# Kernel tuning notes

Measured on AMD Instinct MI355X. Metric: run time of the kernel, lower is better.

The kernel has to match this reference:

```python
import jax, jax.numpy as jnp
import numpy as np

P = 7      # local_patch_size
H = 6      # heads
DH = 30    # dim_head


def setup_inputs() -> dict:
    key = jax.random.key(0)
    ks = jax.random.split(key, 5)
    b, dim, L = 16, 180, 14336
    inner = H * DH  # 180
    fmap = jax.random.normal(ks[0], (b, dim, L), dtype=jnp.float32)
    Wq = jax.random.normal(ks[1], (inner, dim), dtype=jnp.float32) * 0.05
    Wkv = jax.random.normal(ks[2], (2 * inner, dim), dtype=jnp.float32) * 0.05
    Wo = jax.random.normal(ks[3], (dim, inner), dtype=jnp.float32) * 0.05
    bo = jax.random.normal(ks[4], (dim,), dtype=jnp.float32) * 0.05
    return {"fmap": fmap, "Wq": Wq, "Wkv": Wkv, "Wo": Wo, "bo": bo}


def reference(fmap, Wq, Wkv, Wo, bo):
    b, c, L = fmap.shape
    l = L // P
    scale = DH ** -0.5
    # 'b c (l p) -> b c l p' windows
    x = fmap.reshape(b, c, l, P)
    # pointwise (kernel-1) conv projections
    q = jnp.einsum('ec,bclp->belp', Wq, x)
    kv = jnp.einsum('ec,bclp->belp', Wkv, x)
    k, v = jnp.split(kv, 2, axis=1)

    def split_heads(t):
        # (b, h*d, l, p) -> (b, l, h, p, d)
        return t.reshape(b, H, DH, l, P).transpose(0, 3, 1, 4, 2)

    q, k, v = map(split_heads, (q, k, v))
    dots = jnp.einsum('blhid,blhjd->blhij', q, k) * scale  # per-window 7x7 scores
    attn = jax.nn.softmax(dots, axis=-1)
    out = jnp.einsum('blhij,blhjd->blhid', attn, v)  # (b, l, h, p, d)
    # '(b l h) p d -> b (h d) (l p)'
    out = out.transpose(0, 2, 4, 1, 3).reshape(b, H * DH, l * P)
    return jnp.einsum('oe,bel->bol', Wo, out) + bo[None, :, None]
```

## Files before the change

### kernel.cpp

```cpp
#include <hip/hip_runtime.h>
#include <stdint.h>

namespace {

constexpr int DIM  = 180;
constexpr int LL   = 14336;
constexpr int B    = 16;
constexpr int T    = 56;
constexpr int NCH  = 256;
constexpr int EQKV = 540;

constexpr int QTS  = 392;
constexpr int KOFF = 192;
constexpr int QT_U16  = T * QTS;
constexpr int VT_U16  = 24 * 512;
constexpr int XSS     = 200;
constexpr int XS_U16  = 32 * XSS;
constexpr int LDS_U16 = QT_U16 + VT_U16 + XS_U16;

typedef __attribute__((ext_vector_type(8))) short bf16x8;
typedef __attribute__((ext_vector_type(4))) float f32x4;

union Frag { bf16x8 v; uint32_t u[4]; unsigned short s[8]; };

__device__ __forceinline__ unsigned short f2b(float f) {
  uint32_t u = __builtin_bit_cast(uint32_t, f);
  u = (u + 0x7fffu + ((u >> 16) & 1u)) >> 16;
  return (unsigned short)u;
}
__device__ __forceinline__ uint32_t pack2(float lo, float hi) {
  return (uint32_t)f2b(lo) | ((uint32_t)f2b(hi) << 16);
}
__device__ __forceinline__ f32x4 zero4() { f32x4 z = {0.f,0.f,0.f,0.f}; return z; }

}

__global__ __launch_bounds__(1024) void la_prep(
    const float* __restrict__ Wq, const float* __restrict__ Wkv,
    const float* __restrict__ Wo, unsigned short* __restrict__ wqkv_b,
    unsigned short* __restrict__ wo_h) {
  const int idx = (int)(blockIdx.x * 1024 + threadIdx.x);
  if (idx < 576 * 192) {
    const int e = idx / 192, c = idx - e * 192;
    float v = 0.f;
    if (e < EQKV && c < DIM)
      v = (e < DIM) ? Wq[e * DIM + c] : Wkv[(size_t)(e - DIM) * DIM + c];
    wqkv_b[idx] = f2b(v);
  } else {
    const int k = idx - 576 * 192;
    if (k < 192 * 192) {
      const int o = k / 192, cc = k - o * 192;
      const int h = cc >> 5, d = cc & 31;
      float v = 0.f;
      if (o < DIM && d < 30) v = Wo[o * DIM + h * 30 + d];
      wo_h[k] = f2b(v);
    }
  }
}

__global__ __launch_bounds__(512, 4) void la_main(
    const float* __restrict__ fmap, const unsigned short* __restrict__ wqkv,
    const unsigned short* __restrict__ wo_h, const float* __restrict__ bo,
    float* __restrict__ out) {
  __shared__ __align__(16) unsigned short lds[LDS_U16];
  unsigned short* qt = lds;
  unsigned short* vt = lds + QT_U16;
  unsigned short* xs = lds + QT_U16 + VT_U16;

  const int tid  = (int)threadIdx.x;
  const int wave = tid >> 6;
  const int lane = tid & 63;
  const int l15  = lane & 15;
  const int g    = lane >> 4;

  const int bi    = (int)blockIdx.x;
  const int b     = bi >> 8;
  const int chunk = bi & 255;
  const int t0    = chunk * T;

  const unsigned short* wA = wqkv + (size_t)l15 * 192 + g * 8;

#pragma unroll
  for (int it = 0; it < 3; ++it)
    ((uint4*)vt)[tid + it * 512] = make_uint4(0u, 0u, 0u, 0u);

#pragma unroll
  for (int ph = 0; ph < 2; ++ph) {
    const int tb = ph * 32;
#pragma unroll
    for (int it = 0; it < 3; ++it) {
      const int idx = tid + it * 512;
      const int c  = idx >> 3;
      const int tq = (idx & 7) * 4;
      float4 v = {0.f, 0.f, 0.f, 0.f};
      if (c < DIM && (tb + tq) < T)
        v = *(const float4*)(fmap + (size_t)(b * DIM + c) * LL + t0 + tb + tq);
      unsigned short* xr = xs + tq * XSS + c;
      xr[0 * XSS] = f2b(v.x);
      xr[1 * XSS] = f2b(v.y);
      xr[2 * XSS] = f2b(v.z);
      xr[3 * XSS] = f2b(v.w);
    }
    bf16x8 An[6];
#pragma unroll
    for (int ks = 0; ks < 6; ++ks)
      An[ks] = *(const bf16x8*)(wA + (size_t)(wave * 16) * 192 + ks * 32);
    __syncthreads();
    bf16x8 b0[6], b1[6];
#pragma unroll
    for (int ks = 0; ks < 6; ++ks) {
      b0[ks] = *(const bf16x8*)(xs + l15 * XSS + ks * 32 + g * 8);
      b1[ks] = *(const bf16x8*)(xs + (16 + l15) * XSS + ks * 32 + g * 8);
    }
    int mt = wave;
#pragma unroll 5
    for (int it = 0; it < 5; ++it) {
      if (mt < 36) {
        bf16x8 A[6];
#pragma unroll
        for (int ks = 0; ks < 6; ++ks) A[ks] = An[ks];
        const int mtn = mt + 8;
        if (mtn < 36) {
#pragma unroll
          for (int ks = 0; ks < 6; ++ks)
            An[ks] = *(const bf16x8*)(wA + (size_t)(mtn * 16) * 192 + ks * 32);
        }
        f32x4 a0 = zero4(), a1 = zero4();
#pragma unroll
        for (int ks = 0; ks < 6; ++ks) {
          a0 = __builtin_amdgcn_mfma_f32_16x16x32_bf16(A[ks], b0[ks], a0, 0, 0, 0);
          a1 = __builtin_amdgcn_mfma_f32_16x16x32_bf16(A[ks], b1[ks], a1, 0, 0, 0);
        }
        const int e0 = mt * 16 + g * 4;
        if (e0 < EQKV) {
#pragma unroll
          for (int nt = 0; nt < 2; ++nt) {
            const f32x4 A4 = nt ? a1 : a0;
            const int t = tb + nt * 16 + l15;
            if (t < T) {
              if (e0 < 360) {
                unsigned short* qrow = qt + t * QTS;
#pragma unroll
                for (int pr = 0; pr < 2; ++pr) {
                  const int e = e0 + 2 * pr;
                  int col;
                  if (e < 180) { const int h = e / 30; col = e + 2 * h; }
                  else { const int rr = e - 180; const int h = rr / 30; col = KOFF + rr + 2 * h; }
                  *(uint32_t*)(qrow + col) = pack2(A4[2 * pr], A4[2 * pr + 1]);
                }
              } else {
                const int wp = t / 14, jp = t - wp * 14;
#pragma unroll
                for (int r = 0; r < 4; ++r) {
                  const int rr = e0 - 360 + r;
                  const int h = rr / 30, d = rr - 30 * h;
                  vt[((wp * 6 + h) << 9) + (d << 4) + jp] = f2b(A4[r]);
                }
              }
            }
          }
        }
      }
      mt += 8;
    }
    __syncthreads();
  }

  const float scale = 0.18257418583505536f;
#pragma unroll
  for (int u = 0; u < 3; ++u) {
    const int unit = wave * 3 + u;
    const int wp = unit / 6, h = unit - wp * 6;
    const int twb = wp * 14;
    const int arow = twb + l15;
    const unsigned short* rowp = qt + ((arow < T) ? arow : (T - 1)) * QTS;
    Frag A, Bq;
    A.v  = *(const bf16x8*)(rowp + KOFF + (h << 5) + (g << 3));
    Bq.v = *(const bf16x8*)(rowp + (h << 5) + (g << 3));
    if (g == 3) { A.u[3] = 0; Bq.u[3] = 0; }
    const f32x4 s = __builtin_amdgcn_mfma_f32_16x16x32_bf16(A.v, Bq.v, zero4(), 0, 0, 0);
    float p[4];
    float mx = -3e38f;
#pragma unroll
    for (int r = 0; r < 4; ++r) {
      const int j = (g << 2) + r;
      const bool valid = (l15 < 7) ? (j < 7) : (j >= 7 && j < 14);
      p[r] = valid ? s[r] : -3e38f;
      mx = fmaxf(mx, p[r]);
    }
    mx = fmaxf(mx, __shfl_xor(mx, 16));
    mx = fmaxf(mx, __shfl_xor(mx, 32));
    float sum = 0.f;
#pragma unroll
    for (int r = 0; r < 4; ++r) {
      p[r] = __expf(scale * (p[r] - mx));
      sum += p[r];
    }
    sum += __shfl_xor(sum, 16);
    sum += __shfl_xor(sum, 32);
    const float inv = 1.f / sum;
#pragma unroll
    for (int r = 0; r < 4; ++r) p[r] *= inv;
    const uint32_t pk0 = pack2(p[0], p[1]);
    const uint32_t pk1 = pack2(p[2], p[3]);
    const int s0 = l15 + ((g & 1) << 5);
    Frag PA;
    PA.u[0] = __shfl(pk0, s0);
    PA.u[1] = __shfl(pk1, s0);
    PA.u[2] = __shfl(pk0, s0 + 16);
    PA.u[3] = __shfl(pk1, s0 + 16);
    if (g >= 2) { PA.u[0] = 0; PA.u[1] = 0; PA.u[2] = 0; PA.u[3] = 0; }
    const unsigned short* vtb = vt + ((wp * 6 + h) << 9);
    const bf16x8 V0 = *(const bf16x8*)(vtb + (l15 << 4) + (g << 3));
    const bf16x8 V1 = *(const bf16x8*)(vtb + ((16 + l15) << 4) + (g << 3));
    const f32x4 o0 = __builtin_amdgcn_mfma_f32_16x16x32_bf16(PA.v, V0, zero4(), 0, 0, 0);
    const f32x4 o1 = __builtin_amdgcn_mfma_f32_16x16x32_bf16(PA.v, V1, zero4(), 0, 0, 0);
#pragma unroll
    for (int r = 0; r < 4; ++r) {
      const int irow = (g << 2) + r;
      if (irow < 14) {
        unsigned short* orow = qt + (twb + irow) * QTS + (h << 5);
        orow[l15] = f2b(o0[r]);
        orow[16 + l15] = f2b(o1[r]);
      }
    }
  }
  __syncthreads();

  {
    const int n3 = wave & 3;
    const int m3 = (wave >> 2) * 6;
    const int tc  = n3 * 16 + l15;
    const int trd = (tc < T) ? tc : (T - 1);
    bf16x8 bq[6];
#pragma unroll
    for (int ks = 0; ks < 6; ++ks)
      bq[ks] = *(const bf16x8*)(qt + trd * QTS + ks * 32 + g * 8);
    const unsigned short* wO = wo_h + (size_t)l15 * 192 + g * 8;
    bf16x8 An[6];
#pragma unroll
    for (int ks = 0; ks < 6; ++ks)
      An[ks] = *(const bf16x8*)(wO + (size_t)(m3 * 16) * 192 + ks * 32);
#pragma unroll 6
    for (int k6 = 0; k6 < 6; ++k6) {
      const int m = m3 + k6;
      bf16x8 A[6];
#pragma unroll
      for (int ks = 0; ks < 6; ++ks) A[ks] = An[ks];
      if (k6 < 5) {
#pragma unroll
        for (int ks = 0; ks < 6; ++ks)
          An[ks] = *(const bf16x8*)(wO + (size_t)((m + 1) * 16) * 192 + ks * 32);
      }
      f32x4 acc = zero4();
#pragma unroll
      for (int ks = 0; ks < 6; ++ks)
        acc = __builtin_amdgcn_mfma_f32_16x16x32_bf16(A[ks], bq[ks], acc, 0, 0, 0);
      if (tc < T) {
#pragma unroll
        for (int r = 0; r < 4; ++r) {
          const int o = m * 16 + g * 4 + r;
          if (o < DIM)
            out[(size_t)(b * DIM + o) * LL + t0 + tc] = acc[r] + bo[o];
        }
      }
    }
  }
}

extern "C" void kernel_launch(void* const* d_in, const int* in_sizes, int n_in,
                              void* d_out, int out_size, void* d_ws, size_t ws_size,
                              hipStream_t stream) {
  const float* fmap = (const float*)d_in[0];
  const float* Wq   = (const float*)d_in[1];
  const float* Wkv  = (const float*)d_in[2];
  const float* Wo   = (const float*)d_in[3];
  const float* bo   = (const float*)d_in[4];
  float* o = (float*)d_out;

  unsigned short* wqkv_b = (unsigned short*)d_ws;
  unsigned short* wo_h   = wqkv_b + 576 * 192;

  const int prep_elems = 576 * 192 + 192 * 192;
  hipLaunchKernelGGL(la_prep, dim3((prep_elems + 1023) / 1024), dim3(1024), 0,
                     stream, Wq, Wkv, Wo, wqkv_b, wo_h);
  hipLaunchKernelGGL(la_main, dim3(B * NCH), dim3(512), 0, stream,
                     fmap, wqkv_b, wo_h, bo, o);
}
```

Before: 448.9 us.

## Halve per-block token chunk to raise occupancy and rebalance wave work mapping

Each block now handles 28 tokens (two windows) instead of 56, doubling the grid to 512 chunks per batch and shrinking LDS so more blocks fit per CU (launch bounds min blocks raised to 6). The QKV projection is restructured from two phases with register double-buffered weight prefetch to a single phase where each wave does 9 M-tiles for one 16-token N-tile, loading weights directly. The per-head division is replaced with a multiply-shift, and bf16 conversion now uses the HIP intrinsic. It trades more total weight reads from L2 (weights reloaded per smaller block) and idle waves in attention for higher occupancy and latency hiding.

```diff
diff --git a/kernel.cpp b/kernel.cpp
--- a/kernel.cpp
+++ b/kernel.cpp
@@ -1,4 +1,5 @@
 #include <hip/hip_runtime.h>
+#include <hip/hip_bf16.h>
 #include <stdint.h>
 
 namespace {
@@ -6,14 +7,14 @@
 constexpr int DIM  = 180;
 constexpr int LL   = 14336;
 constexpr int B    = 16;
-constexpr int T    = 56;
-constexpr int NCH  = 256;
+constexpr int T    = 28;
+constexpr int NCH  = 512;
 constexpr int EQKV = 540;
 
 constexpr int QTS  = 392;
 constexpr int KOFF = 192;
 constexpr int QT_U16  = T * QTS;
-constexpr int VT_U16  = 24 * 512;
+constexpr int VT_U16  = 12 * 512;
 constexpr int XSS     = 200;
 constexpr int XS_U16  = 32 * XSS;
 constexpr int LDS_U16 = QT_U16 + VT_U16 + XS_U16;
@@ -24,9 +25,8 @@
 union Frag { bf16x8 v; uint32_t u[4]; unsigned short s[8]; };
 
 __device__ __forceinline__ unsigned short f2b(float f) {
-  uint32_t u = __builtin_bit_cast(uint32_t, f);
-  u = (u + 0x7fffu + ((u >> 16) & 1u)) >> 16;
-  return (unsigned short)u;
+  const __hip_bfloat16 h = __float2bfloat16(f);
+  return __builtin_bit_cast(unsigned short, h);
 }
 __device__ __forceinline__ uint32_t pack2(float lo, float hi) {
   return (uint32_t)f2b(lo) | ((uint32_t)f2b(hi) << 16);
@@ -58,7 +58,7 @@
   }
 }
 
-__global__ __launch_bounds__(512, 4) void la_main(
+__global__ __launch_bounds__(512, 6) void la_main(
     const float* __restrict__ fmap, const unsigned short* __restrict__ wqkv,
     const unsigned short* __restrict__ wo_h, const float* __restrict__ bo,
     float* __restrict__ out) {
@@ -74,162 +74,142 @@
   const int g    = lane >> 4;
 
   const int bi    = (int)blockIdx.x;
-  const int b     = bi >> 8;
-  const int chunk = bi & 255;
+  const int b     = bi >> 9;
+  const int chunk = bi & 511;
   const int t0    = chunk * T;
 
-  const unsigned short* wA = wqkv + (size_t)l15 * 192 + g * 8;
-
-#pragma unroll
-  for (int it = 0; it < 3; ++it)
-    ((uint4*)vt)[tid + it * 512] = make_uint4(0u, 0u, 0u, 0u);
-
-#pragma unroll
-  for (int ph = 0; ph < 2; ++ph) {
-    const int tb = ph * 32;
-#pragma unroll
-    for (int it = 0; it < 3; ++it) {
-      const int idx = tid + it * 512;
-      const int c  = idx >> 3;
-      const int tq = (idx & 7) * 4;
-      float4 v = {0.f, 0.f, 0.f, 0.f};
-      if (c < DIM && (tb + tq) < T)
-        v = *(const float4*)(fmap + (size_t)(b * DIM + c) * LL + t0 + tb + tq);
-      unsigned short* xr = xs + tq * XSS + c;
-      xr[0 * XSS] = f2b(v.x);
-      xr[1 * XSS] = f2b(v.y);
-      xr[2 * XSS] = f2b(v.z);
-      xr[3 * XSS] = f2b(v.w);
-    }
-    bf16x8 An[6];
+  {
+    uint4* vt4 = (uint4*)vt;
+    for (int i = tid; i < 768; i += 512) vt4[i] = make_uint4(0u, 0u, 0u, 0u);
+  }
+#pragma unroll
+  for (int it = 0; it < 3; ++it) {
+    const int idx = tid + it * 512;
+    const int c  = idx >> 3;
+    const int tq = (idx & 7) * 4;
+    float4 v = {0.f, 0.f, 0.f, 0.f};
+    if (c < DIM && tq < T)
+      v = *(const float4*)(fmap + (size_t)(b * DIM + c) * LL + t0 + tq);
+    unsigned short* xr = xs + tq * XSS + c;
+    xr[0 * XSS] = f2b(v.x);
+    xr[1 * XSS] = f2b(v.y);
+    xr[2 * XSS] = f2b(v.z);
+    xr[3 * XSS] = f2b(v.w);
+  }
+  __syncthreads();
+
+  {
+    const int nw = wave & 1;
+    const int m9 = (wave >> 1) * 9;
+    bf16x8 bf[6];
 #pragma unroll
     for (int ks = 0; ks < 6; ++ks)
-      An[ks] = *(const bf16x8*)(wA + (size_t)(wave * 16) * 192 + ks * 32);
-    __syncthreads();
-    bf16x8 b0[6], b1[6];
-#pragma unroll
-    for (int ks = 0; ks < 6; ++ks) {
-      b0[ks] = *(const bf16x8*)(xs + l15 * XSS + ks * 32 + g * 8);
-      b1[ks] = *(const bf16x8*)(xs + (16 + l15) * XSS + ks * 32 + g * 8);
-    }
-    int mt = wave;
-#pragma unroll 5
-    for (int it = 0; it < 5; ++it) {
-      if (mt < 36) {
-        bf16x8 A[6];
-#pragma unroll
-        for (int ks = 0; ks < 6; ++ks) A[ks] = An[ks];
-        const int mtn = mt + 8;
-        if (mtn < 36) {
-#pragma unroll
-          for (int ks = 0; ks < 6; ++ks)
-            An[ks] = *(const bf16x8*)(wA + (size_t)(mtn * 16) * 192 + ks * 32);
-        }
-        f32x4 a0 = zero4(), a1 = zero4();
-#pragma unroll
-        for (int ks = 0; ks < 6; ++ks) {
-          a0 = __builtin_amdgcn_mfma_f32_16x16x32_bf16(A[ks], b0[ks], a0, 0, 0, 0);
-          a1 = __builtin_amdgcn_mfma_f32_16x16x32_bf16(A[ks], b1[ks], a1, 0, 0, 0);
-        }
-        const int e0 = mt * 16 + g * 4;
-        if (e0 < EQKV) {
-#pragma unroll
-          for (int nt = 0; nt < 2; ++nt) {
-            const f32x4 A4 = nt ? a1 : a0;
-            const int t = tb + nt * 16 + l15;
-            if (t < T) {
-              if (e0 < 360) {
-                unsigned short* qrow = qt + t * QTS;
-#pragma unroll
-                for (int pr = 0; pr < 2; ++pr) {
-                  const int e = e0 + 2 * pr;
-                  int col;
-                  if (e < 180) { const int h = e / 30; col = e + 2 * h; }
-                  else { const int rr = e - 180; const int h = rr / 30; col = KOFF + rr + 2 * h; }
-                  *(uint32_t*)(qrow + col) = pack2(A4[2 * pr], A4[2 * pr + 1]);
-                }
-              } else {
-                const int wp = t / 14, jp = t - wp * 14;
-#pragma unroll
-                for (int r = 0; r < 4; ++r) {
-                  const int rr = e0 - 360 + r;
-                  const int h = rr / 30, d = rr - 30 * h;
-                  vt[((wp * 6 + h) << 9) + (d << 4) + jp] = f2b(A4[r]);
-                }
-              }
-            }
+      bf[ks] = *(const bf16x8*)(xs + (nw * 16 + l15) * XSS + ks * 32 + g * 8);
+    const unsigned short* wA = wqkv + (size_t)l15 * 192 + g * 8;
+    const int t = nw * 16 + l15;
+#pragma unroll 3
+    for (int k9 = 0; k9 < 9; ++k9) {
+      const int mt = m9 + k9;
+      f32x4 acc = zero4();
+#pragma unroll
+      for (int ks = 0; ks < 6; ++ks) {
+        const bf16x8 a = *(const bf16x8*)(wA + (size_t)(mt * 16) * 192 + ks * 32);
+        acc = __builtin_amdgcn_mfma_f32_16x16x32_bf16(a, bf[ks], acc, 0, 0, 0);
+      }
+      const int e0 = mt * 16 + g * 4;
+      if (t < T && e0 < EQKV) {
+        if (e0 < 360) {
+          unsigned short* qrow = qt + t * QTS;
+#pragma unroll
+          for (int pr = 0; pr < 2; ++pr) {
+            const int e = e0 + 2 * pr;
+            int col;
+            if (e < 180) { const int h = (e * 34953) >> 20; col = e + 2 * h; }
+            else { const int rr = e - 180; const int h = (rr * 34953) >> 20; col = KOFF + rr + 2 * h; }
+            *(uint32_t*)(qrow + col) = pack2(acc[2 * pr], acc[2 * pr + 1]);
+          }
+        } else {
+          const int wp = (t >= 14) ? 1 : 0;
+          const int jp = t - wp * 14;
+#pragma unroll
+          for (int r = 0; r < 4; ++r) {
+            const int rr = e0 - 360 + r;
+            const int h = (rr * 34953) >> 20;
+            const int d = rr - h * 30;
+            vt[((wp * 6 + h) << 9) + (d << 4) + jp] = f2b(acc[r]);
           }
         }
       }
-      mt += 8;
-    }
-    __syncthreads();
-  }
+    }
+  }
+  __syncthreads();
 
   const float scale = 0.18257418583505536f;
-#pragma unroll
-  for (int u = 0; u < 3; ++u) {
-    const int unit = wave * 3 + u;
-    const int wp = unit / 6, h = unit - wp * 6;
-    const int twb = wp * 14;
-    const int arow = twb + l15;
-    const unsigned short* rowp = qt + ((arow < T) ? arow : (T - 1)) * QTS;
-    Frag A, Bq;
-    A.v  = *(const bf16x8*)(rowp + KOFF + (h << 5) + (g << 3));
-    Bq.v = *(const bf16x8*)(rowp + (h << 5) + (g << 3));
-    if (g == 3) { A.u[3] = 0; Bq.u[3] = 0; }
-    const f32x4 s = __builtin_amdgcn_mfma_f32_16x16x32_bf16(A.v, Bq.v, zero4(), 0, 0, 0);
-    float p[4];
-    float mx = -3e38f;
-#pragma unroll
-    for (int r = 0; r < 4; ++r) {
-      const int j = (g << 2) + r;
-      const bool valid = (l15 < 7) ? (j < 7) : (j >= 7 && j < 14);
-      p[r] = valid ? s[r] : -3e38f;
-      mx = fmaxf(mx, p[r]);
-    }
-    mx = fmaxf(mx, __shfl_xor(mx, 16));
-    mx = fmaxf(mx, __shfl_xor(mx, 32));
-    float sum = 0.f;
-#pragma unroll
-    for (int r = 0; r < 4; ++r) {
-      p[r] = __expf(scale * (p[r] - mx));
-      sum += p[r];
-    }
-    sum += __shfl_xor(sum, 16);
-    sum += __shfl_xor(sum, 32);
-    const float inv = 1.f / sum;
-#pragma unroll
-    for (int r = 0; r < 4; ++r) p[r] *= inv;
-    const uint32_t pk0 = pack2(p[0], p[1]);
-    const uint32_t pk1 = pack2(p[2], p[3]);
-    const int s0 = l15 + ((g & 1) << 5);
-    Frag PA;
-    PA.u[0] = __shfl(pk0, s0);
-    PA.u[1] = __shfl(pk1, s0);
-    PA.u[2] = __shfl(pk0, s0 + 16);
-    PA.u[3] = __shfl(pk1, s0 + 16);
-    if (g >= 2) { PA.u[0] = 0; PA.u[1] = 0; PA.u[2] = 0; PA.u[3] = 0; }
-    const unsigned short* vtb = vt + ((wp * 6 + h) << 9);
-    const bf16x8 V0 = *(const bf16x8*)(vtb + (l15 << 4) + (g << 3));
-    const bf16x8 V1 = *(const bf16x8*)(vtb + ((16 + l15) << 4) + (g << 3));
-    const f32x4 o0 = __builtin_amdgcn_mfma_f32_16x16x32_bf16(PA.v, V0, zero4(), 0, 0, 0);
-    const f32x4 o1 = __builtin_amdgcn_mfma_f32_16x16x32_bf16(PA.v, V1, zero4(), 0, 0, 0);
-#pragma unroll
-    for (int r = 0; r < 4; ++r) {
-      const int irow = (g << 2) + r;
-      if (irow < 14) {
-        unsigned short* orow = qt + (twb + irow) * QTS + (h << 5);
-        orow[l15] = f2b(o0[r]);
-        orow[16 + l15] = f2b(o1[r]);
+  if (wave < 6) {
+#pragma unroll
+    for (int u = 0; u < 2; ++u) {
+      const int unit = wave * 2 + u;
+      const int wp = unit / 6, h = unit - wp * 6;
+      const int twb = wp * 14;
+      const int arow = twb + l15;
+      const unsigned short* rowp = qt + ((arow < T) ? arow : (T - 1)) * QTS;
+      Frag A, Bq;
+      A.v  = *(const bf16x8*)(rowp + KOFF + (h << 5) + (g << 3));
+      Bq.v = *(const bf16x8*)(rowp + (h << 5) + (g << 3));
+      if (g == 3) { A.u[3] = 0; Bq.u[3] = 0; }
+      const f32x4 s = __builtin_amdgcn_mfma_f32_16x16x32_bf16(A.v, Bq.v, zero4(), 0, 0, 0);
+      float p[4];
+      float mx = -3e38f;
+#pragma unroll
+      for (int r = 0; r < 4; ++r) {
+        const int j = (g << 2) + r;
+        const bool valid = (l15 < 7) ? (j < 7) : (j >= 7 && j < 14);
+        p[r] = valid ? s[r] : -3e38f;
+        mx = fmaxf(mx, p[r]);
+      }
+      mx = fmaxf(mx, __shfl_xor(mx, 16));
+      mx = fmaxf(mx, __shfl_xor(mx, 32));
+      float sum = 0.f;
+#pragma unroll
+      for (int r = 0; r < 4; ++r) {
+        p[r] = __expf(scale * (p[r] - mx));
+        sum += p[r];
+      }
+      sum += __shfl_xor(sum, 16);
+      sum += __shfl_xor(sum, 32);
+      const float inv = 1.f / sum;
+#pragma unroll
+      for (int r = 0; r < 4; ++r) p[r] *= inv;
+      const uint32_t pk0 = pack2(p[0], p[1]);
+      const uint32_t pk1 = pack2(p[2], p[3]);
+      const int s0 = l15 + ((g & 1) << 5);
+      Frag PA;
+      PA.u[0] = __shfl(pk0, s0);
+      PA.u[1] = __shfl(pk1, s0);
+      PA.u[2] = __shfl(pk0, s0 + 16);
+      PA.u[3] = __shfl(pk1, s0 + 16);
+      if (g >= 2) { PA.u[0] = 0; PA.u[1] = 0; PA.u[2] = 0; PA.u[3] = 0; }
+      const unsigned short* vtb = vt + ((wp * 6 + h) << 9);
+      const bf16x8 V0 = *(const bf16x8*)(vtb + (l15 << 4) + (g << 3));
+      const bf16x8 V1 = *(const bf16x8*)(vtb + ((16 + l15) << 4) + (g << 3));
+      const f32x4 o0 = __builtin_amdgcn_mfma_f32_16x16x32_bf16(PA.v, V0, zero4(), 0, 0, 0);
+      const f32x4 o1 = __builtin_amdgcn_mfma_f32_16x16x32_bf16(PA.v, V1, zero4(), 0, 0, 0);
+#pragma unroll
+      for (int r = 0; r < 4; ++r) {
+        const int irow = (g << 2) + r;
+        if (irow < 14) {
+          unsigned short* orow = qt + (twb + irow) * QTS + (h << 5);
+          orow[l15] = f2b(o0[r]);
+          orow[16 + l15] = f2b(o1[r]);
+        }
       }
     }
   }
   __syncthreads();
 
   {
-    const int n3 = wave & 3;
-    const int m3 = (wave >> 2) * 6;
+    const int n3 = wave & 1;
+    const int m3 = (wave >> 1) * 3;
     const int tc  = n3 * 16 + l15;
     const int trd = (tc < T) ? tc : (T - 1);
     bf16x8 bq[6];
@@ -237,25 +217,15 @@
     for (int ks = 0; ks < 6; ++ks)
       bq[ks] = *(const bf16x8*)(qt + trd * QTS + ks * 32 + g * 8);
     const unsigned short* wO = wo_h + (size_t)l15 * 192 + g * 8;
-    bf16x8 An[6];
-#pragma unroll
-    for (int ks = 0; ks < 6; ++ks)
-      An[ks] = *(const bf16x8*)(wO + (size_t)(m3 * 16) * 192 + ks * 32);
-#pragma unroll 6
-    for (int k6 = 0; k6 < 6; ++k6) {
+#pragma unroll 3
+    for (int k6 = 0; k6 < 3; ++k6) {
       const int m = m3 + k6;
-      bf16x8 A[6];
-#pragma unroll
-      for (int ks = 0; ks < 6; ++ks) A[ks] = An[ks];
-      if (k6 < 5) {
-#pragma unroll
-        for (int ks = 0; ks < 6; ++ks)
-          An[ks] = *(const bf16x8*)(wO + (size_t)((m + 1) * 16) * 192 + ks * 32);
-      }
       f32x4 acc = zero4();
 #pragma unroll
-      for (int ks = 0; ks < 6; ++ks)
-        acc = __builtin_amdgcn_mfma_f32_16x16x32_bf16(A[ks], bq[ks], acc, 0, 0, 0);
+      for (int ks = 0; ks < 6; ++ks) {
+        const bf16x8 a = *(const bf16x8*)(wO + (size_t)(m * 16) * 192 + ks * 32);
+        acc = __builtin_amdgcn_mfma_f32_16x16x32_bf16(a, bq[ks], acc, 0, 0, 0);
+      }
       if (tc < T) {
 #pragma unroll
         for (int r = 0; r < 4; ++r) {
```

New measurement: 597.6 us. 33.1% more time.
